# Kernel optimization log

Hardware: AMD Instinct MI355X
Metric: run time of the kernel (lower is better)

## Reference

```python
import jax, jax.numpy as jnp
import numpy as np

EPS = 1e-7  # utils.add_dummy(eps=True) dummy value


def setup_inputs() -> dict:
    key = jax.random.key(0)
    ks = jax.random.split(key, 8)
    n_mentions, emb = 8192, 1024
    batch, n_ants, pw_emb = 1024, 50, 64
    pair_emb = 3 * emb + pw_emb  # 3136
    hidden = 1024
    return {
        "all_mentions": jax.random.normal(ks[0], (n_mentions, emb), jnp.float32),
        "mentions_batch": jax.random.normal(ks[1], (batch, emb), jnp.float32),
        "pw_batch": jax.random.normal(ks[2], (batch, n_ants, pw_emb), jnp.float32),
        "top_rough_scores_batch": jax.random.normal(ks[3], (batch, n_ants), jnp.float32),
        "W1": jax.random.normal(ks[4], (pair_emb, hidden), jnp.float32) * 0.02,
        "b1": jnp.zeros((hidden,), jnp.float32),
        "W_out": jax.random.normal(ks[5], (hidden, 1), jnp.float32) * 0.02,
        "b_out": jnp.zeros((1,), jnp.float32),
        "top_indices_batch": jax.random.randint(ks[6], (batch, n_ants), 0, n_mentions, jnp.int64),
    }


def reference(all_mentions, mentions_batch, pw_batch, top_rough_scores_batch,
              W1, b1, W_out, b_out, top_indices_batch):
    # gather antecedent embeddings: [batch, n_ants, emb]
    b_mentions = all_mentions[top_indices_batch]
    a_mentions = jnp.broadcast_to(mentions_batch[:, None, :], b_mentions.shape)
    # pair matrix: [batch, n_ants, 3*emb + pw_emb]
    pair = jnp.concatenate([a_mentions, b_mentions, a_mentions * b_mentions, pw_batch], axis=2)
    # FFNN: Linear -> LeakyReLU (dropout is identity in eval) -> Linear(->1)
    h = jax.nn.leaky_relu(jnp.einsum("bnf,fh->bnh", pair, W1) + b1, negative_slope=0.01)
    ffnn = (jnp.einsum("bnh,ho->bno", h, W_out) + b_out)[..., 0]  # [batch, n_ants]
    scores = top_rough_scores_batch + ffnn
    dummy = jnp.full((scores.shape[0], 1), EPS, scores.dtype)
    return jnp.concatenate([dummy, scores], axis=1)  # [batch, n_ants + 1]
```

## Files before the change

kernel.cpp:

```cpp
#include <hip/hip_runtime.h>
#include <cstdint>


typedef short short8 __attribute__((ext_vector_type(8)));
typedef float f32x4 __attribute__((ext_vector_type(4)));

#define BT_STRIDE 100352
#define MT_STRIDE 32768
#define PT_STRIDE 34816

static __device__ __forceinline__ unsigned short f2bf(float x) {
  union { float f; unsigned u; } v; v.f = x;
  unsigned r = v.u + 0x7fffu + ((v.u >> 16) & 1u);
  return (unsigned short)(r >> 16);
}
static __device__ __forceinline__ float bf2f(unsigned short u) {
  union { unsigned u; float f; } v; v.u = ((unsigned)u) << 16;
  return v.f;
}

__global__ void k_packW(const float* __restrict__ W1, unsigned short* __restrict__ BtAll) {
  __shared__ float t[64][65];
  int k0 = blockIdx.x * 64, n0 = blockIdx.y * 64;
  int c = threadIdx.x & 63, r4 = threadIdx.x >> 6;
#pragma unroll
  for (int rr = 0; rr < 16; ++rr) {
    int r = rr * 4 + r4;
    t[r][c] = W1[(size_t)(k0 + r) * 1024 + n0 + c];
  }
  __syncthreads();
#pragma unroll
  for (int qq = 0; qq < 2; ++qq) {
    int q = threadIdx.x * 2 + qq;
    int cc = q >> 3, rg = q & 7;
    short8 v;
#pragma unroll
    for (int e = 0; e < 8; ++e) v[e] = (short)f2bf(t[rg * 8 + e][cc]);
    int ct = (n0 + cc) >> 4;
    int kc = (k0 >> 5) + (rg >> 2);
    int ln = (cc & 15) + ((rg & 3) << 4);
    *(short8*)((char*)BtAll + (size_t)ct * BT_STRIDE + kc * 1024 + ln * 16) = v;
  }
}

__global__ void k_cvt(const float* __restrict__ s, unsigned short* __restrict__ d, int n4) {
  int i = blockIdx.x * 256 + threadIdx.x;
  if (i < n4) {
    float4 v = ((const float4*)s)[i];
    ushort4 o; o.x = f2bf(v.x); o.y = f2bf(v.y); o.z = f2bf(v.z); o.w = f2bf(v.w);
    ((ushort4*)d)[i] = o;
  }
}

__global__ void k_packM(const float* __restrict__ am, const float* __restrict__ allm,
                        unsigned short* __restrict__ Mt) {
  int rt = blockIdx.x, t = threadIdx.x;
  const float* S = (rt < 512) ? (allm + (size_t)rt * 16 * 1024)
                              : (am + (size_t)(rt - 512) * 16 * 1024);
  int pf = t & 15, oct = (t >> 4) & 3, kcl = t >> 6;
  const float* row = S + (size_t)pf * 1024;
  char* dst = (char*)Mt + (size_t)rt * MT_STRIDE + (t & 63) * 16;
#pragma unroll
  for (int pass = 0; pass < 8; ++pass) {
    int kc = pass * 4 + kcl;
    int k = kc * 32 + oct * 8;
    float4 v0 = *(const float4*)(row + k);
    float4 v1 = *(const float4*)(row + k + 4);
    short8 o;
    o[0] = (short)f2bf(v0.x); o[1] = (short)f2bf(v0.y);
    o[2] = (short)f2bf(v0.z); o[3] = (short)f2bf(v0.w);
    o[4] = (short)f2bf(v1.x); o[5] = (short)f2bf(v1.y);
    o[6] = (short)f2bf(v1.z); o[7] = (short)f2bf(v1.w);
    *(short8*)(dst + kc * 1024) = o;
  }
}

__global__ void k_pairs(const unsigned short* __restrict__ Abm,
                        const unsigned short* __restrict__ Aball,
                        const float* __restrict__ pw, const int* __restrict__ idx,
                        unsigned short* __restrict__ Pt) {
  __shared__ int g16[16];
  int rt = blockIdx.x, t = threadIdx.x;
  if (t < 16) g16[t] = idx[rt * 16 + t];
  __syncthreads();
  int pf = t & 15, oct = (t >> 4) & 3, kcl = t >> 6;
  int p = rt * 16 + pf;
  const unsigned short* arow = Abm + (size_t)(p / 50) * 1024;
  const unsigned short* brow = Aball + (size_t)g16[pf] * 1024;
  char* dst = (char*)Pt + (size_t)rt * PT_STRIDE + (t & 63) * 16;
#pragma unroll
  for (int pass = 0; pass < 8; ++pass) {
    int kc = pass * 4 + kcl;
    int k = kc * 32 + oct * 8;
    short8 a8 = *(const short8*)(arow + k);
    short8 b8 = *(const short8*)(brow + k);
    short8 o;
#pragma unroll
    for (int e = 0; e < 8; ++e)
      o[e] = (short)f2bf(bf2f((unsigned short)a8[e]) * bf2f((unsigned short)b8[e]));
    *(short8*)(dst + kc * 1024) = o;
  }
  if (t < 128) {
    int kc = 32 + (t >> 6);
    int kpw = (t >> 6) * 32 + oct * 8;
    const float* prow = pw + (size_t)p * 64;
    float4 v0 = *(const float4*)(prow + kpw);
    float4 v1 = *(const float4*)(prow + kpw + 4);
    short8 o;
    o[0] = (short)f2bf(v0.x); o[1] = (short)f2bf(v0.y);
    o[2] = (short)f2bf(v0.z); o[3] = (short)f2bf(v0.w);
    o[4] = (short)f2bf(v1.x); o[5] = (short)f2bf(v1.y);
    o[6] = (short)f2bf(v1.z); o[7] = (short)f2bf(v1.w);
    *(short8*)(dst + kc * 1024) = o;
  }
}

template <int MODE>
__global__ __launch_bounds__(256, 2) void k_gt(
    const unsigned short* __restrict__ At, const unsigned short* __restrict__ BtAll,
    float* __restrict__ C, float* __restrict__ partial,
    const float* __restrict__ Hab, const float* __restrict__ b1,
    const float* __restrict__ Wout, const int* __restrict__ idx) {
  constexpr int NKC = MODE ? 34 : 32;
  constexpr int A_STRIDE = MODE ? PT_STRIDE : MT_STRIDE;
  int tid = threadIdx.x, lane = tid & 63, wave = tid >> 6;
  int llo = lane & 15, lhi = lane >> 4;
  int id = blockIdx.x;
  int x, y;
  if (MODE == 1) {
    int r = id >> 3;
    x = (id & 7) * 25 + (r >> 3);
    y = r & 7;
  } else {
    x = id >> 3;
    y = id & 7;
  }
  int kcoff = MODE ? 64 : ((x < 32) ? 32 : 0);
  int row0 = x * 256 + wave * 64;
  int n0 = y * 128;
  const char* pa = (const char*)At + (size_t)(row0 >> 4) * A_STRIDE + lane * 16;
  const char* pb = (const char*)BtAll + (size_t)(n0 >> 4) * BT_STRIDE +
                   (size_t)kcoff * 1024 + lane * 16;

  f32x4 acc[4][8] = {};
  short8 aA[4], bA[8], aB[4], bB[8];
#pragma unroll
  for (int m = 0; m < 4; ++m) aA[m] = *(const short8*)(pa + (size_t)m * A_STRIDE);
#pragma unroll
  for (int n = 0; n < 8; ++n) bA[n] = *(const short8*)(pb + (size_t)n * BT_STRIDE);
  for (int kt = 0; kt < NKC; kt += 2) {
#pragma unroll
    for (int m = 0; m < 4; ++m)
      aB[m] = *(const short8*)(pa + (size_t)m * A_STRIDE + (kt + 1) * 1024);
#pragma unroll
    for (int n = 0; n < 8; ++n)
      bB[n] = *(const short8*)(pb + (size_t)n * BT_STRIDE + (kt + 1) * 1024);
#pragma unroll
    for (int m = 0; m < 4; ++m)
#pragma unroll
      for (int n = 0; n < 8; ++n)
        acc[m][n] = __builtin_amdgcn_mfma_f32_16x16x32_bf16(aA[m], bA[n], acc[m][n], 0, 0, 0);
    if (kt + 2 < NKC) {
#pragma unroll
      for (int m = 0; m < 4; ++m)
        aA[m] = *(const short8*)(pa + (size_t)m * A_STRIDE + (kt + 2) * 1024);
#pragma unroll
      for (int n = 0; n < 8; ++n)
        bA[n] = *(const short8*)(pb + (size_t)n * BT_STRIDE + (kt + 2) * 1024);
    }
#pragma unroll
    for (int m = 0; m < 4; ++m)
#pragma unroll
      for (int n = 0; n < 8; ++n)
        acc[m][n] = __builtin_amdgcn_mfma_f32_16x16x32_bf16(aB[m], bB[n], acc[m][n], 0, 0, 0);
  }

  if (MODE == 0) {
#pragma unroll
    for (int m = 0; m < 4; ++m)
#pragma unroll
      for (int i = 0; i < 4; ++i) {
        int row = row0 + m * 16 + lhi * 4 + i;
#pragma unroll
        for (int n = 0; n < 8; ++n)
          C[(size_t)row * 1024 + n0 + n * 16 + llo] = acc[m][n][i];
      }
  } else {
    float b1v[8], wov[8];
    int coln[8];
#pragma unroll
    for (int n = 0; n < 8; ++n) {
      coln[n] = n0 + n * 16 + llo;
      b1v[n] = b1[coln[n]];
      wov[n] = Wout[coln[n]];
    }
#pragma unroll
    for (int m = 0; m < 4; ++m)
#pragma unroll
      for (int i = 0; i < 4; ++i) {
        int p = row0 + m * 16 + lhi * 4 + i;
        int bb = p / 50;
        int gg = idx[p];
        const float* Har = Hab + (size_t)(8192 + bb) * 1024;
        const float* Hbr = Hab + (size_t)gg * 1024;
        float s0 = 0.f, s1 = 0.f;
#pragma unroll
        for (int n = 0; n < 4; ++n) {
          float h = acc[m][n][i] + Har[coln[n]] + Hbr[coln[n]] + b1v[n];
          h = h > 0.f ? h : 0.01f * h;
          s0 += h * wov[n];
        }
#pragma unroll
        for (int n = 4; n < 8; ++n) {
          float h = acc[m][n][i] + Har[coln[n]] + Hbr[coln[n]] + b1v[n];
          h = h > 0.f ? h : 0.01f * h;
          s1 += h * wov[n];
        }
        s0 += __shfl_xor(s0, 1, 64);
        s0 += __shfl_xor(s0, 2, 64);
        s0 += __shfl_xor(s0, 4, 64);
        s0 += __shfl_xor(s0, 8, 64);
        s1 += __shfl_xor(s1, 1, 64);
        s1 += __shfl_xor(s1, 2, 64);
        s1 += __shfl_xor(s1, 4, 64);
        s1 += __shfl_xor(s1, 8, 64);
        if (llo == 0) {
          partial[(size_t)p * 16 + y * 2 + 0] = s0;
          partial[(size_t)p * 16 + y * 2 + 1] = s1;
        }
      }
  }
}

__global__ void k_final(const float* __restrict__ partial, const float* __restrict__ rough,
                        const float* __restrict__ bout, float* __restrict__ out) {
  int t = blockIdx.x * 256 + threadIdx.x;
  if (t < 51200) {
    float s = rough[t] + bout[0];
    const float* pp = partial + (size_t)t * 16;
#pragma unroll
    for (int c = 0; c < 16; ++c) s += pp[c];
    out[(size_t)(t / 50) * 51 + 1 + (t % 50)] = s;
  }
  if (t < 1024) out[(size_t)t * 51] = 1e-7f;
}

extern "C" void kernel_launch(void* const* d_in, const int* in_sizes, int n_in,
                              void* d_out, int out_size, void* d_ws, size_t ws_size,
                              hipStream_t stream) {
  (void)in_sizes; (void)n_in; (void)out_size;
  const float* allm  = (const float*)d_in[0];
  const float* am    = (const float*)d_in[1];
  const float* pw    = (const float*)d_in[2];
  const float* rough = (const float*)d_in[3];
  const float* W1    = (const float*)d_in[4];
  const float* b1    = (const float*)d_in[5];
  const float* Wout  = (const float*)d_in[6];
  const float* bout  = (const float*)d_in[7];
  const int*   idx   = (const int*)d_in[8];
  float* out = (float*)d_out;

  char* w = (char*)d_ws;
  unsigned short* BtAll = (unsigned short*)w; w += (size_t)64 * BT_STRIDE;
  unsigned short* Mt    = (unsigned short*)w; w += (size_t)576 * MT_STRIDE;
  unsigned short* Abm   = (unsigned short*)w; w += (size_t)1024 * 1024 * 2;
  unsigned short* Aball = (unsigned short*)w; w += (size_t)8192 * 1024 * 2;
  unsigned short* Pt    = (unsigned short*)w; w += (size_t)3200 * PT_STRIDE;
  float* Hab            = (float*)w;          w += (size_t)9216 * 1024 * 4;
  float* part           = (float*)w;          w += (size_t)51200 * 16 * 4;
  size_t need = (size_t)(w - (char*)d_ws);
  if (ws_size < need) return;

  k_packW<<<dim3(49, 16), 256, 0, stream>>>(W1, BtAll);
  k_cvt<<<dim3(1024), 256, 0, stream>>>(am, Abm, 1024 * 1024 / 4);
  k_cvt<<<dim3(8192), 256, 0, stream>>>(allm, Aball, 8192 * 1024 / 4);
  k_packM<<<dim3(576), 256, 0, stream>>>(am, allm, Mt);
  k_pairs<<<dim3(3200), 256, 0, stream>>>(Abm, Aball, pw, idx, Pt);
  k_gt<0><<<dim3(288), 256, 0, stream>>>(Mt, BtAll, Hab, nullptr,
                                         nullptr, nullptr, nullptr, nullptr);
  k_gt<1><<<dim3(1600), 256, 0, stream>>>(Pt, BtAll, nullptr, part,
                                          Hab, b1, Wout, idx);
  k_final<<<dim3(200), 256, 0, stream>>>(part, rough, bout, out);
}
```

Measured before the change: 256.4 us.

## Stage A-operand tiles through LDS via direct global-to-LDS loads

```diff
diff --git a/kernel.cpp b/kernel.cpp
--- a/kernel.cpp
+++ b/kernel.cpp
@@ -17,6 +17,12 @@
 static __device__ __forceinline__ float bf2f(unsigned short u) {
   union { unsigned u; float f; } v; v.u = ((unsigned)u) << 16;
   return v.f;
+}
+
+static __device__ __forceinline__ void gload_lds16(const void* g, void* lds) {
+  __builtin_amdgcn_global_load_lds(
+      (const __attribute__((address_space(1))) void*)(unsigned long long)(uintptr_t)g,
+      (__attribute__((address_space(3))) void*)(unsigned)(uintptr_t)lds, 16, 0, 0);
 }
 
 __global__ void k_packW(const float* __restrict__ W1, unsigned short* __restrict__ BtAll) {
@@ -123,6 +129,7 @@
     const float* __restrict__ Wout, const int* __restrict__ idx) {
   constexpr int NKC = MODE ? 34 : 32;
   constexpr int A_STRIDE = MODE ? PT_STRIDE : MT_STRIDE;
+  __shared__ char AL[4][2][4096];
   int tid = threadIdx.x, lane = tid & 63, wave = tid >> 6;
   int llo = lane & 15, lhi = lane >> 4;
   int id = blockIdx.x;
@@ -141,39 +148,56 @@
   const char* pa = (const char*)At + (size_t)(row0 >> 4) * A_STRIDE + lane * 16;
   const char* pb = (const char*)BtAll + (size_t)(n0 >> 4) * BT_STRIDE +
                    (size_t)kcoff * 1024 + lane * 16;
+  char* myA = &AL[wave][0][0];
 
   f32x4 acc[4][8] = {};
-  short8 aA[4], bA[8], aB[4], bB[8];
-#pragma unroll
-  for (int m = 0; m < 4; ++m) aA[m] = *(const short8*)(pa + (size_t)m * A_STRIDE);
-#pragma unroll
-  for (int n = 0; n < 8; ++n) bA[n] = *(const short8*)(pb + (size_t)n * BT_STRIDE);
-  for (int kt = 0; kt < NKC; kt += 2) {
-#pragma unroll
-    for (int m = 0; m < 4; ++m)
-      aB[m] = *(const short8*)(pa + (size_t)m * A_STRIDE + (kt + 1) * 1024);
-#pragma unroll
-    for (int n = 0; n < 8; ++n)
-      bB[n] = *(const short8*)(pb + (size_t)n * BT_STRIDE + (kt + 1) * 1024);
-#pragma unroll
-    for (int m = 0; m < 4; ++m)
-#pragma unroll
-      for (int n = 0; n < 8; ++n)
-        acc[m][n] = __builtin_amdgcn_mfma_f32_16x16x32_bf16(aA[m], bA[n], acc[m][n], 0, 0, 0);
-    if (kt + 2 < NKC) {
-#pragma unroll
-      for (int m = 0; m < 4; ++m)
-        aA[m] = *(const short8*)(pa + (size_t)m * A_STRIDE + (kt + 2) * 1024);
-#pragma unroll
-      for (int n = 0; n < 8; ++n)
-        bA[n] = *(const short8*)(pb + (size_t)n * BT_STRIDE + (kt + 2) * 1024);
-    }
-#pragma unroll
-    for (int m = 0; m < 4; ++m)
-#pragma unroll
-      for (int n = 0; n < 8; ++n)
-        acc[m][n] = __builtin_amdgcn_mfma_f32_16x16x32_bf16(aB[m], bB[n], acc[m][n], 0, 0, 0);
-  }
+  short8 breg0[8], breg1[8];
+
+#pragma unroll
+  for (int m = 0; m < 4; ++m)
+    gload_lds16(pa + (size_t)m * A_STRIDE, myA + m * 1024 + lane * 16);
+#pragma unroll
+  for (int n = 0; n < 8; ++n)
+    breg0[n] = *(const short8*)(pb + (size_t)n * BT_STRIDE);
+  __builtin_amdgcn_sched_barrier(0);
+#pragma unroll
+  for (int m = 0; m < 4; ++m)
+    gload_lds16(pa + (size_t)m * A_STRIDE + 1024, myA + 4096 + m * 1024 + lane * 16);
+#pragma unroll
+  for (int n = 0; n < 8; ++n)
+    breg1[n] = *(const short8*)(pb + (size_t)n * BT_STRIDE + 1024);
+  __builtin_amdgcn_sched_barrier(0);
+
+#define GT_ITER(KT, PH, BREG)                                                   \
+  {                                                                             \
+    if ((KT) < NKC - 1) asm volatile("s_waitcnt vmcnt(12)" ::: "memory");       \
+    else                asm volatile("s_waitcnt vmcnt(0)" ::: "memory");        \
+    short8 af[4];                                                               \
+    _Pragma("unroll")                                                           \
+    for (int m = 0; m < 4; ++m)                                                 \
+      af[m] = *(const short8*)(myA + (PH) * 4096 + m * 1024 + lane * 16);       \
+    _Pragma("unroll")                                                           \
+    for (int m = 0; m < 4; ++m)                                                 \
+      _Pragma("unroll")                                                         \
+      for (int n = 0; n < 8; ++n)                                               \
+        acc[m][n] = __builtin_amdgcn_mfma_f32_16x16x32_bf16(af[m], BREG[n],     \
+                                                            acc[m][n], 0, 0, 0);\
+    if ((KT) + 2 < NKC) {                                                       \
+      _Pragma("unroll")                                                         \
+      for (int m = 0; m < 4; ++m)                                               \
+        gload_lds16(pa + (size_t)m * A_STRIDE + ((KT) + 2) * 1024,              \
+                    myA + (PH) * 4096 + m * 1024 + lane * 16);                  \
+      _Pragma("unroll")                                                         \
+      for (int n = 0; n < 8; ++n)                                               \
+        BREG[n] = *(const short8*)(pb + (size_t)n * BT_STRIDE + ((KT) + 2) * 1024);\
+    }                                                                           \
+  }
+
+  for (int kt2 = 0; kt2 < NKC; kt2 += 2) {
+    GT_ITER(kt2, 0, breg0);
+    GT_ITER(kt2 + 1, 1, breg1);
+  }
+#undef GT_ITER
 
   if (MODE == 0) {
 #pragma unroll
```

Result: slower. 263.7 us (+2.8%).
